# Kernel optimization log

Measured on AMD Instinct MI355X. Metric: run time of the kernel, lower is better.

## Reference

```python
import jax, jax.numpy as jnp
import numpy as np

EPS = 1e-8
BETA = 0.02          # bisector-band sharpness
ALPHA_UNION = 8.0    # exp-union strength
W_MIN, W_MAX = 0.005, 0.5
RAW_TEMP = 5.0       # width squash temperature
REL_TEMP = 0.05      # seed-relevance softmax temperature
A_MIN, A_MAX = 0.5, 2.0  # anisotropy eigenvalue range


def setup_inputs() -> dict:
    key = jax.random.key(0)
    k1, k2, k3, k4, k5 = jax.random.split(key, 5)
    N, S = 65536, 32
    return {
        "points_uv": jax.random.uniform(k1, (N, 2), dtype=jnp.float32),
        "seeds_raw": jax.random.uniform(k2, (S, 2), dtype=jnp.float32),
        "w_raw": jax.random.normal(k3, (1,), dtype=jnp.float32),
        "theta": jax.random.normal(k4, (S,), dtype=jnp.float32),
        "a_raw": jax.random.normal(k5, (S,), dtype=jnp.float32),
    }


def _metric_matrices(theta, a_raw):
    # anisotropic 2x2 SPD metrics M_s = R^T diag(a, 1/a) R
    t = jnp.tanh(a_raw)
    a = 0.5 * (A_MAX - A_MIN) * t + 0.5 * (A_MAX + A_MIN)  # (S,)
    c, s = jnp.cos(theta), jnp.sin(theta)
    R = jnp.stack([jnp.stack([c, -s], -1), jnp.stack([s, c], -1)], -2)  # (S,2,2)
    dvec = jnp.stack([a, 1.0 / (a + EPS)], -1)  # (S,2)
    return jnp.einsum("ska,sk,skb->sab", R, dvec, R)  # (S,2,2)


def reference(points_uv, seeds_raw, w_raw, theta, a_raw):
    S = seeds_raw.shape[0]
    # half-thickness around the Voronoi bisector
    w = W_MIN + (W_MAX - W_MIN) * jax.nn.sigmoid(w_raw[0] / RAW_TEMP)
    M = _metric_matrices(theta, a_raw)  # (S,2,2)

    # point-to-seed diffs with periodic wrapping on both u and v
    diff = points_uv[:, None, :] - seeds_raw[None, :, :]  # (N,S,2)
    diff = diff - jnp.round(diff)

    # anisotropic distances d_i(x) = sqrt(diff^T M_i diff)
    d = jnp.sqrt(jnp.einsum("nsa,sab,nsb->ns", diff, M, diff) + EPS)  # (N,S)

    # soft seed relevance -> soft pair weights P_ij (upper triangular, normalized)
    w_soft = jax.nn.softmax(-d / REL_TEMP, axis=1)  # (N,S)
    pair = w_soft[:, :, None] * w_soft[:, None, :]  # (N,S,S)
    mask = jnp.triu(jnp.ones((S, S), dtype=points_uv.dtype), k=1)
    pair = pair * mask
    P = pair / (pair.sum(axis=(1, 2), keepdims=True) + EPS)

    # bisector band: B_ij = sigmoid((w - |d_i - d_j|_smooth) / beta)
    Delta = d[:, :, None] - d[:, None, :]  # (N,S,S)
    abs_smooth = jnp.sqrt(Delta * Delta + EPS)
    B = jax.nn.sigmoid((w - abs_smooth) / BETA)

    # union over i<j pairs: rho = 1 - exp(-alpha * sum S_ij)
    S_sum = jnp.sum(P * B, axis=(1, 2))  # (N,)
    rho = 1.0 - jnp.exp(-ALPHA_UNION * S_sum)
    return rho
```

## Files before the change

kernel.cpp:

```cpp
#include <hip/hip_runtime.h>
#include <math.h>


#define LOG2E  1.4426950408889634f
#define EPSF   1e-8f
#define TSCALE 4096.0f
#define TAB_N  4160
#define BLOCK  512
#define PPB    64
#define SSTR   40

__device__ __forceinline__ float tabB(const char* tb, unsigned a, unsigned b) {
    const unsigned hi = a > b ? a : b;
    const unsigned lo = a > b ? b : a;
    return *(const float*)(tb + (hi - lo));
}

__global__ __launch_bounds__(BLOCK) void voronoi_v5(
    const float* __restrict__ points,
    const float* __restrict__ seeds,
    const float* __restrict__ w_raw,
    const float* __restrict__ theta,
    const float* __restrict__ a_raw,
    float* __restrict__ out,
    int N)
{
    __shared__ float    s_tab[TAB_N];
    __shared__ unsigned s_di[PPB * SSTR];
    __shared__ float    s_ww[PPB * SSTR];
    __shared__ float    s_su[32], s_sv[32], s_m00[32], s_m01[32], s_m11[32];

    const int t = threadIdx.x;

    const float wr = w_raw[0];
    const float sg = __builtin_amdgcn_rcpf(1.0f + exp2f(wr * (-LOG2E / 5.0f)));
    const float w  = 0.005f + 0.495f * sg;

    if (t < 32) {
        const float x  = a_raw[t];
        const float z  = exp2f(2.0f * LOG2E * x);
        const float th = (z - 1.0f) * __builtin_amdgcn_rcpf(z + 1.0f);
        const float a  = 0.75f * th + 1.25f;
        const float ia = __builtin_amdgcn_rcpf(a + EPSF);
        const float cs = __cosf(theta[t]);
        const float sn = __sinf(theta[t]);
        const float S2 = TSCALE * TSCALE;
        s_m00[t] = (a * cs * cs + ia * sn * sn) * S2;
        s_m01[t] = (2.0f * cs * sn * (ia - a)) * S2;
        s_m11[t] = (a * sn * sn + ia * cs * cs) * S2;
        s_su[t]  = seeds[2 * t];
        s_sv[t]  = seeds[2 * t + 1];
    }
    {
        const float kC = (50.0f * LOG2E) / TSCALE;
        const float kB = -w * (50.0f * LOG2E);
        for (int k = t; k < TAB_N; k += BLOCK) {
            const float y = exp2f(fmaf((float)k, kC, kB));
            s_tab[k] = __builtin_amdgcn_rcpf(1.0f + y);
        }
    }
    __syncthreads();

    const int pb = t >> 3;
    const int g  = t & 7;
    const int s0 = g * 4;
    const int p  = blockIdx.x * PPB + pb;
    if (p >= N) return;

    const float4 su4  = *(const float4*)&s_su[s0];
    const float4 sv4  = *(const float4*)&s_sv[s0];
    const float4 m004 = *(const float4*)&s_m00[s0];
    const float4 m014 = *(const float4*)&s_m01[s0];
    const float4 m114 = *(const float4*)&s_m11[s0];

    const float2 uv = ((const float2*)points)[p];
    const float u = uv.x, v = uv.y;

    const float EPS_Q = 1e-8f * TSCALE * TSCALE;
    float4 d4;
#define DIST(SU, SV, M00, M01, M11, OUTD)                                  \
    {                                                                      \
        float du = u - (SU); du -= rintf(du);                              \
        float dv = v - (SV); dv -= rintf(dv);                              \
        float q = fmaf(du * du, (M00),                                     \
                  fmaf(du * dv, (M01),                                     \
                  fmaf(dv * dv, (M11), EPS_Q)));                           \
        (OUTD) = sqrtf(q);                                                 \
    }
    DIST(su4.x, sv4.x, m004.x, m014.x, m114.x, d4.x)
    DIST(su4.y, sv4.y, m004.y, m014.y, m114.y, d4.y)
    DIST(su4.z, sv4.z, m004.z, m014.z, m114.z, d4.z)
    DIST(su4.w, sv4.w, m004.w, m014.w, m114.w, d4.w)

    const float cE = -(20.0f * LOG2E) / TSCALE;
    float4 e4;
    e4.x = exp2f(d4.x * cE);
    e4.y = exp2f(d4.y * cE);
    e4.z = exp2f(d4.z * cE);
    e4.w = exp2f(d4.w * cE);
    float Z = (e4.x + e4.y) + (e4.z + e4.w);
    Z += __shfl_xor(Z, 1, 64);
    Z += __shfl_xor(Z, 2, 64);
    Z += __shfl_xor(Z, 4, 64);
    const float rcpZ = __builtin_amdgcn_rcpf(Z);
    float4 w4;
    w4.x = e4.x * rcpZ; w4.y = e4.y * rcpZ;
    w4.z = e4.z * rcpZ; w4.w = e4.w * rcpZ;
    float sumsq = w4.x * w4.x;
    sumsq = fmaf(w4.y, w4.y, sumsq);
    sumsq = fmaf(w4.z, w4.z, sumsq);
    sumsq = fmaf(w4.w, w4.w, sumsq);

    uint4 ii;
    ii.x = ((unsigned)(d4.x + 0.5f)) << 2;
    ii.y = ((unsigned)(d4.y + 0.5f)) << 2;
    ii.z = ((unsigned)(d4.z + 0.5f)) << 2;
    ii.w = ((unsigned)(d4.w + 0.5f)) << 2;

    unsigned* db = &s_di[pb * SSTR];
    float*    wb = &s_ww[pb * SSTR];
    *(uint4*) (db + s0) = ii;
    *(float4*)(wb + s0) = w4;

    const char* tb = (const char*)s_tab;

    float b0, b1, b2, b3;
    b0 =      tabB(tb, ii.x, ii.y) * w4.y;
    b0 = fmaf(tabB(tb, ii.x, ii.z), w4.z, b0);
    b0 = fmaf(tabB(tb, ii.x, ii.w), w4.w, b0);
    b1 =      tabB(tb, ii.y, ii.z) * w4.z;
    b1 = fmaf(tabB(tb, ii.y, ii.w), w4.w, b1);
    b2 =      tabB(tb, ii.z, ii.w) * w4.w;
    b3 = 0.0f;

#define ROT(R, HALF)                                                       \
    {                                                                      \
        const int gj = ((g + (R)) & 7) * 4;                                \
        const uint4  ij = *(const uint4*) (db + gj);                       \
        float4 wj = *(const float4*)(wb + gj);                             \
        if (HALF) { wj.x *= 0.5f; wj.y *= 0.5f; wj.z *= 0.5f; wj.w *= 0.5f; } \
        b0 = fmaf(tabB(tb, ii.x, ij.x), wj.x, b0);                         \
        b0 = fmaf(tabB(tb, ii.x, ij.y), wj.y, b0);                         \
        b0 = fmaf(tabB(tb, ii.x, ij.z), wj.z, b0);                         \
        b0 = fmaf(tabB(tb, ii.x, ij.w), wj.w, b0);                         \
        b1 = fmaf(tabB(tb, ii.y, ij.x), wj.x, b1);                         \
        b1 = fmaf(tabB(tb, ii.y, ij.y), wj.y, b1);                         \
        b1 = fmaf(tabB(tb, ii.y, ij.z), wj.z, b1);                         \
        b1 = fmaf(tabB(tb, ii.y, ij.w), wj.w, b1);                         \
        b2 = fmaf(tabB(tb, ii.z, ij.x), wj.x, b2);                         \
        b2 = fmaf(tabB(tb, ii.z, ij.y), wj.y, b2);                         \
        b2 = fmaf(tabB(tb, ii.z, ij.z), wj.z, b2);                         \
        b2 = fmaf(tabB(tb, ii.z, ij.w), wj.w, b2);                         \
        b3 = fmaf(tabB(tb, ii.w, ij.x), wj.x, b3);                         \
        b3 = fmaf(tabB(tb, ii.w, ij.y), wj.y, b3);                         \
        b3 = fmaf(tabB(tb, ii.w, ij.z), wj.z, b3);                         \
        b3 = fmaf(tabB(tb, ii.w, ij.w), wj.w, b3);                         \
    }
    ROT(1, 0)
    ROT(2, 0)
    ROT(3, 0)
    ROT(4, 1)

    float accb = w4.x * b0;
    accb = fmaf(w4.y, b1, accb);
    accb = fmaf(w4.z, b2, accb);
    accb = fmaf(w4.w, b3, accb);

    float nb = accb, sq = sumsq;
    nb += __shfl_xor(nb, 1, 64);  sq += __shfl_xor(sq, 1, 64);
    nb += __shfl_xor(nb, 2, 64);  sq += __shfl_xor(sq, 2, 64);
    nb += __shfl_xor(nb, 4, 64);  sq += __shfl_xor(sq, 4, 64);

    const float den   = fmaxf(0.5f * (1.0f - sq), 0.0f) + EPSF;
    const float ratio = nb * __builtin_amdgcn_rcpf(den);
    const float rho   = 1.0f - exp2f(ratio * (-8.0f * LOG2E));
    if (g == 0) out[p] = rho;
}

extern "C" void kernel_launch(void* const* d_in, const int* in_sizes, int n_in,
                              void* d_out, int out_size, void* d_ws, size_t ws_size,
                              hipStream_t stream) {
    const float* points = (const float*)d_in[0];
    const float* seeds  = (const float*)d_in[1];
    const float* w_raw  = (const float*)d_in[2];
    const float* theta  = (const float*)d_in[3];
    const float* a_raw  = (const float*)d_in[4];
    float* out = (float*)d_out;

    const int N = in_sizes[0] / 2;
    const int grid = (N + PPB - 1) / PPB;

    voronoi_v5<<<grid, BLOCK, 0, stream>>>(points, seeds, w_raw, theta, a_raw,
                                           out, N);
}
```

Measured before the change: 16.85 us.

## Shrink sigmoid table to band around w and halve symmetric rotation work

The lookup table is cut to a clamped window of indices around the band centre w, on the assumption that the sigmoid is flat outside that window. This reduces the per-block table initialization and LDS footprint. The fourth rotation step is now done by only half the lanes instead of all lanes with halved weights, which removes duplicated pair work but adds divergence. Launch bounds ask for higher occupancy. Clamping index differences adds two min/max ops per lookup and approximates the table outside the window.

```diff
diff --git a/kernel.cpp b/kernel.cpp
--- a/kernel.cpp
+++ b/kernel.cpp
@@ -4,19 +4,14 @@
 
 #define LOG2E  1.4426950408889634f
 #define EPSF   1e-8f
-#define TSCALE 4096.0f
-#define TAB_N  4160
+#define TSC    4096.0f
+#define TAB_N  2816
+#define HBAND  750
 #define BLOCK  512
 #define PPB    64
 #define SSTR   40
 
-__device__ __forceinline__ float tabB(const char* tb, unsigned a, unsigned b) {
-    const unsigned hi = a > b ? a : b;
-    const unsigned lo = a > b ? b : a;
-    return *(const float*)(tb + (hi - lo));
-}
-
-__global__ __launch_bounds__(BLOCK) void voronoi_v5(
+__global__ __launch_bounds__(BLOCK, 8) void voronoi_v7(
     const float* __restrict__ points,
     const float* __restrict__ seeds,
     const float* __restrict__ w_raw,
@@ -26,7 +21,7 @@
     int N)
 {
     __shared__ float    s_tab[TAB_N];
-    __shared__ unsigned s_di[PPB * SSTR];
+    __shared__ unsigned s_ii[PPB * SSTR];
     __shared__ float    s_ww[PPB * SSTR];
     __shared__ float    s_su[32], s_sv[32], s_m00[32], s_m01[32], s_m11[32];
 
@@ -35,6 +30,10 @@
     const float wr = w_raw[0];
     const float sg = __builtin_amdgcn_rcpf(1.0f + exp2f(wr * (-LOG2E / 5.0f)));
     const float w  = 0.005f + 0.495f * sg;
+
+    const int icent = (int)(w * TSC + 0.5f);
+    const int T1B   = (icent > HBAND ? icent - HBAND : 0) << 2;
+    const int T2B   = (icent + HBAND) << 2;
 
     if (t < 32) {
         const float x  = a_raw[t];
@@ -44,7 +43,7 @@
         const float ia = __builtin_amdgcn_rcpf(a + EPSF);
         const float cs = __cosf(theta[t]);
         const float sn = __sinf(theta[t]);
-        const float S2 = TSCALE * TSCALE;
+        const float S2 = TSC * TSC;
         s_m00[t] = (a * cs * cs + ia * sn * sn) * S2;
         s_m01[t] = (2.0f * cs * sn * (ia - a)) * S2;
         s_m11[t] = (a * sn * sn + ia * cs * cs) * S2;
@@ -52,8 +51,9 @@
         s_sv[t]  = seeds[2 * t + 1];
     }
     {
-        const float kC = (50.0f * LOG2E) / TSCALE;
+        const float kC = (50.0f * LOG2E) / TSC;
         const float kB = -w * (50.0f * LOG2E);
+        #pragma unroll
         for (int k = t; k < TAB_N; k += BLOCK) {
             const float y = exp2f(fmaf((float)k, kC, kB));
             s_tab[k] = __builtin_amdgcn_rcpf(1.0f + y);
@@ -76,7 +76,7 @@
     const float2 uv = ((const float2*)points)[p];
     const float u = uv.x, v = uv.y;
 
-    const float EPS_Q = 1e-8f * TSCALE * TSCALE;
+    const float EPS_Q = 1e-8f * TSC * TSC;
     float4 d4;
 #define DIST(SU, SV, M00, M01, M11, OUTD)                                  \
     {                                                                      \
@@ -92,7 +92,7 @@
     DIST(su4.z, sv4.z, m004.z, m014.z, m114.z, d4.z)
     DIST(su4.w, sv4.w, m004.w, m014.w, m114.w, d4.w)
 
-    const float cE = -(20.0f * LOG2E) / TSCALE;
+    const float cE = -(20.0f * LOG2E) / TSC;
     float4 e4;
     e4.x = exp2f(d4.x * cE);
     e4.y = exp2f(d4.y * cE);
@@ -117,49 +117,61 @@
     ii.z = ((unsigned)(d4.z + 0.5f)) << 2;
     ii.w = ((unsigned)(d4.w + 0.5f)) << 2;
 
-    unsigned* db = &s_di[pb * SSTR];
+    unsigned* db = &s_ii[pb * SSTR];
     float*    wb = &s_ww[pb * SSTR];
     *(uint4*) (db + s0) = ii;
     *(float4*)(wb + s0) = w4;
 
     const char* tb = (const char*)s_tab;
 
+#define TBODY(IA, IB, WJ, ACC)                                             \
+    {                                                                      \
+        const unsigned hi = (IA) > (IB) ? (IA) : (IB);                     \
+        const unsigned lo = (IA) > (IB) ? (IB) : (IA);                     \
+        int diff = (int)(hi - lo);                                         \
+        diff = diff > T1B ? diff : T1B;                                    \
+        diff = diff < T2B ? diff : T2B;                                    \
+        const float B = *(const float*)(tb + diff);                        \
+        (ACC) = fmaf((WJ), B, (ACC));                                      \
+    }
+
     float b0, b1, b2, b3;
-    b0 =      tabB(tb, ii.x, ii.y) * w4.y;
-    b0 = fmaf(tabB(tb, ii.x, ii.z), w4.z, b0);
-    b0 = fmaf(tabB(tb, ii.x, ii.w), w4.w, b0);
-    b1 =      tabB(tb, ii.y, ii.z) * w4.z;
-    b1 = fmaf(tabB(tb, ii.y, ii.w), w4.w, b1);
-    b2 =      tabB(tb, ii.z, ii.w) * w4.w;
-    b3 = 0.0f;
-
-#define ROT(R, HALF)                                                       \
+    b0 = 0.0f; b1 = 0.0f; b2 = 0.0f; b3 = 0.0f;
+    TBODY(ii.x, ii.y, w4.y, b0)
+    TBODY(ii.x, ii.z, w4.z, b0)
+    TBODY(ii.x, ii.w, w4.w, b0)
+    TBODY(ii.y, ii.z, w4.z, b1)
+    TBODY(ii.y, ii.w, w4.w, b1)
+    TBODY(ii.z, ii.w, w4.w, b2)
+
+#define ROT(R)                                                             \
     {                                                                      \
         const int gj = ((g + (R)) & 7) * 4;                                \
         const uint4  ij = *(const uint4*) (db + gj);                       \
-        float4 wj = *(const float4*)(wb + gj);                             \
-        if (HALF) { wj.x *= 0.5f; wj.y *= 0.5f; wj.z *= 0.5f; wj.w *= 0.5f; } \
-        b0 = fmaf(tabB(tb, ii.x, ij.x), wj.x, b0);                         \
-        b0 = fmaf(tabB(tb, ii.x, ij.y), wj.y, b0);                         \
-        b0 = fmaf(tabB(tb, ii.x, ij.z), wj.z, b0);                         \
-        b0 = fmaf(tabB(tb, ii.x, ij.w), wj.w, b0);                         \
-        b1 = fmaf(tabB(tb, ii.y, ij.x), wj.x, b1);                         \
-        b1 = fmaf(tabB(tb, ii.y, ij.y), wj.y, b1);                         \
-        b1 = fmaf(tabB(tb, ii.y, ij.z), wj.z, b1);                         \
-        b1 = fmaf(tabB(tb, ii.y, ij.w), wj.w, b1);                         \
-        b2 = fmaf(tabB(tb, ii.z, ij.x), wj.x, b2);                         \
-        b2 = fmaf(tabB(tb, ii.z, ij.y), wj.y, b2);                         \
-        b2 = fmaf(tabB(tb, ii.z, ij.z), wj.z, b2);                         \
-        b2 = fmaf(tabB(tb, ii.z, ij.w), wj.w, b2);                         \
-        b3 = fmaf(tabB(tb, ii.w, ij.x), wj.x, b3);                         \
-        b3 = fmaf(tabB(tb, ii.w, ij.y), wj.y, b3);                         \
-        b3 = fmaf(tabB(tb, ii.w, ij.z), wj.z, b3);                         \
-        b3 = fmaf(tabB(tb, ii.w, ij.w), wj.w, b3);                         \
-    }
-    ROT(1, 0)
-    ROT(2, 0)
-    ROT(3, 0)
-    ROT(4, 1)
+        const float4 wj = *(const float4*)(wb + gj);                       \
+        TBODY(ii.x, ij.x, wj.x, b0)                                        \
+        TBODY(ii.x, ij.y, wj.y, b0)                                        \
+        TBODY(ii.x, ij.z, wj.z, b0)                                        \
+        TBODY(ii.x, ij.w, wj.w, b0)                                        \
+        TBODY(ii.y, ij.x, wj.x, b1)                                        \
+        TBODY(ii.y, ij.y, wj.y, b1)                                        \
+        TBODY(ii.y, ij.z, wj.z, b1)                                        \
+        TBODY(ii.y, ij.w, wj.w, b1)                                        \
+        TBODY(ii.z, ij.x, wj.x, b2)                                        \
+        TBODY(ii.z, ij.y, wj.y, b2)                                        \
+        TBODY(ii.z, ij.z, wj.z, b2)                                        \
+        TBODY(ii.z, ij.w, wj.w, b2)                                        \
+        TBODY(ii.w, ij.x, wj.x, b3)                                        \
+        TBODY(ii.w, ij.y, wj.y, b3)                                        \
+        TBODY(ii.w, ij.z, wj.z, b3)                                        \
+        TBODY(ii.w, ij.w, wj.w, b3)                                        \
+    }
+    ROT(1)
+    ROT(2)
+    ROT(3)
+    if (g < 4) {
+        ROT(4)
+    }
 
     float accb = w4.x * b0;
     accb = fmaf(w4.y, b1, accb);
@@ -190,6 +202,6 @@
     const int N = in_sizes[0] / 2;
     const int grid = (N + PPB - 1) / PPB;
 
-    voronoi_v5<<<grid, BLOCK, 0, stream>>>(points, seeds, w_raw, theta, a_raw,
+    voronoi_v7<<<grid, BLOCK, 0, stream>>>(points, seeds, w_raw, theta, a_raw,
                                            out, N);
 }
```

Result: faster. 16.49 us (-2.1%).

## Replace sigmoid lookup table with clamped rational tanh approximation

Applied to the files above, without the earlier changes.

Drops the per-block shared-memory sigmoid table and the quantized distance indices, and computes the bisector-band sigmoid directly from a clamped Padé tanh approximation in registers. Distances are stored as floats in shared memory instead of scaled integers. The aim is to remove the table build, its LDS footprint, and random LDS gathers, which should allow more blocks per CU (launch bounds raised to 8). The cost is considerably more ALU work per pair, including a reciprocal, and a small accuracy change from clamping at ±4.6.

```diff
diff --git a/kernel.cpp b/kernel.cpp
--- a/kernel.cpp
+++ b/kernel.cpp
@@ -4,19 +4,11 @@
 
 #define LOG2E  1.4426950408889634f
 #define EPSF   1e-8f
-#define TSCALE 4096.0f
-#define TAB_N  4160
 #define BLOCK  512
 #define PPB    64
 #define SSTR   40
 
-__device__ __forceinline__ float tabB(const char* tb, unsigned a, unsigned b) {
-    const unsigned hi = a > b ? a : b;
-    const unsigned lo = a > b ? b : a;
-    return *(const float*)(tb + (hi - lo));
-}
-
-__global__ __launch_bounds__(BLOCK) void voronoi_v5(
+__global__ __launch_bounds__(BLOCK, 8) void voronoi_v8(
     const float* __restrict__ points,
     const float* __restrict__ seeds,
     const float* __restrict__ w_raw,
@@ -25,16 +17,16 @@
     float* __restrict__ out,
     int N)
 {
-    __shared__ float    s_tab[TAB_N];
-    __shared__ unsigned s_di[PPB * SSTR];
-    __shared__ float    s_ww[PPB * SSTR];
-    __shared__ float    s_su[32], s_sv[32], s_m00[32], s_m01[32], s_m11[32];
+    __shared__ float s_dd[PPB * SSTR];
+    __shared__ float s_ww[PPB * SSTR];
+    __shared__ float s_su[32], s_sv[32], s_m00[32], s_m01[32], s_m11[32];
 
     const int t = threadIdx.x;
 
     const float wr = w_raw[0];
     const float sg = __builtin_amdgcn_rcpf(1.0f + exp2f(wr * (-LOG2E / 5.0f)));
     const float w  = 0.005f + 0.495f * sg;
+    const float wc = w * 25.0f;
 
     if (t < 32) {
         const float x  = a_raw[t];
@@ -44,20 +36,11 @@
         const float ia = __builtin_amdgcn_rcpf(a + EPSF);
         const float cs = __cosf(theta[t]);
         const float sn = __sinf(theta[t]);
-        const float S2 = TSCALE * TSCALE;
-        s_m00[t] = (a * cs * cs + ia * sn * sn) * S2;
-        s_m01[t] = (2.0f * cs * sn * (ia - a)) * S2;
-        s_m11[t] = (a * sn * sn + ia * cs * cs) * S2;
+        s_m00[t] = a * cs * cs + ia * sn * sn;
+        s_m01[t] = 2.0f * cs * sn * (ia - a);
+        s_m11[t] = a * sn * sn + ia * cs * cs;
         s_su[t]  = seeds[2 * t];
         s_sv[t]  = seeds[2 * t + 1];
-    }
-    {
-        const float kC = (50.0f * LOG2E) / TSCALE;
-        const float kB = -w * (50.0f * LOG2E);
-        for (int k = t; k < TAB_N; k += BLOCK) {
-            const float y = exp2f(fmaf((float)k, kC, kB));
-            s_tab[k] = __builtin_amdgcn_rcpf(1.0f + y);
-        }
     }
     __syncthreads();
 
@@ -76,7 +59,6 @@
     const float2 uv = ((const float2*)points)[p];
     const float u = uv.x, v = uv.y;
 
-    const float EPS_Q = 1e-8f * TSCALE * TSCALE;
     float4 d4;
 #define DIST(SU, SV, M00, M01, M11, OUTD)                                  \
     {                                                                      \
@@ -84,7 +66,7 @@
         float dv = v - (SV); dv -= rintf(dv);                              \
         float q = fmaf(du * du, (M00),                                     \
                   fmaf(du * dv, (M01),                                     \
-                  fmaf(dv * dv, (M11), EPS_Q)));                           \
+                  fmaf(dv * dv, (M11), EPSF)));                            \
         (OUTD) = sqrtf(q);                                                 \
     }
     DIST(su4.x, sv4.x, m004.x, m014.x, m114.x, d4.x)
@@ -92,7 +74,7 @@
     DIST(su4.z, sv4.z, m004.z, m014.z, m114.z, d4.z)
     DIST(su4.w, sv4.w, m004.w, m014.w, m114.w, d4.w)
 
-    const float cE = -(20.0f * LOG2E) / TSCALE;
+    const float cE = -20.0f * LOG2E;
     float4 e4;
     e4.x = exp2f(d4.x * cE);
     e4.y = exp2f(d4.y * cE);
@@ -111,50 +93,57 @@
     sumsq = fmaf(w4.z, w4.z, sumsq);
     sumsq = fmaf(w4.w, w4.w, sumsq);
 
-    uint4 ii;
-    ii.x = ((unsigned)(d4.x + 0.5f)) << 2;
-    ii.y = ((unsigned)(d4.y + 0.5f)) << 2;
-    ii.z = ((unsigned)(d4.z + 0.5f)) << 2;
-    ii.w = ((unsigned)(d4.w + 0.5f)) << 2;
-
-    unsigned* db = &s_di[pb * SSTR];
-    float*    wb = &s_ww[pb * SSTR];
-    *(uint4*) (db + s0) = ii;
+    float* db = &s_dd[pb * SSTR];
+    float* wb = &s_ww[pb * SSTR];
+    *(float4*)(db + s0) = d4;
     *(float4*)(wb + s0) = w4;
 
-    const char* tb = (const char*)s_tab;
+#define FBODY(DI, DJ, WJ, ACC)                                             \
+    {                                                                      \
+        const float ab = fabsf((DI) - (DJ));                               \
+        float x = fmaf(ab, -25.0f, wc);                                    \
+        x = fminf(fmaxf(x, -4.6f), 4.6f);                                  \
+        const float tt = x * x;                                            \
+        const float nm = fmaf(fmaf(tt + 378.0f, tt, 17325.0f), tt,         \
+                              135135.0f);                                  \
+        const float dn = fmaf(fmaf(fmaf(28.0f, tt, 3150.0f), tt,           \
+                              62370.0f), tt, 135135.0f);                   \
+        const float xr = x * __builtin_amdgcn_rcpf(dn);                    \
+        const float B  = fmaf(nm * xr, 0.5f, 0.5f);                        \
+        (ACC) = fmaf((WJ), B, (ACC));                                      \
+    }
 
     float b0, b1, b2, b3;
-    b0 =      tabB(tb, ii.x, ii.y) * w4.y;
-    b0 = fmaf(tabB(tb, ii.x, ii.z), w4.z, b0);
-    b0 = fmaf(tabB(tb, ii.x, ii.w), w4.w, b0);
-    b1 =      tabB(tb, ii.y, ii.z) * w4.z;
-    b1 = fmaf(tabB(tb, ii.y, ii.w), w4.w, b1);
-    b2 =      tabB(tb, ii.z, ii.w) * w4.w;
-    b3 = 0.0f;
+    b0 = 0.0f; b1 = 0.0f; b2 = 0.0f; b3 = 0.0f;
+    FBODY(d4.x, d4.y, w4.y, b0)
+    FBODY(d4.x, d4.z, w4.z, b0)
+    FBODY(d4.x, d4.w, w4.w, b0)
+    FBODY(d4.y, d4.z, w4.z, b1)
+    FBODY(d4.y, d4.w, w4.w, b1)
+    FBODY(d4.z, d4.w, w4.w, b2)
 
 #define ROT(R, HALF)                                                       \
     {                                                                      \
         const int gj = ((g + (R)) & 7) * 4;                                \
-        const uint4  ij = *(const uint4*) (db + gj);                       \
+        const float4 dj = *(const float4*)(db + gj);                       \
         float4 wj = *(const float4*)(wb + gj);                             \
         if (HALF) { wj.x *= 0.5f; wj.y *= 0.5f; wj.z *= 0.5f; wj.w *= 0.5f; } \
-        b0 = fmaf(tabB(tb, ii.x, ij.x), wj.x, b0);                         \
-        b0 = fmaf(tabB(tb, ii.x, ij.y), wj.y, b0);                         \
-        b0 = fmaf(tabB(tb, ii.x, ij.z), wj.z, b0);                         \
-        b0 = fmaf(tabB(tb, ii.x, ij.w), wj.w, b0);                         \
-        b1 = fmaf(tabB(tb, ii.y, ij.x), wj.x, b1);                         \
-        b1 = fmaf(tabB(tb, ii.y, ij.y), wj.y, b1);                         \
-        b1 = fmaf(tabB(tb, ii.y, ij.z), wj.z, b1);                         \
-        b1 = fmaf(tabB(tb, ii.y, ij.w), wj.w, b1);                         \
-        b2 = fmaf(tabB(tb, ii.z, ij.x), wj.x, b2);                         \
-        b2 = fmaf(tabB(tb, ii.z, ij.y), wj.y, b2);                         \
-        b2 = fmaf(tabB(tb, ii.z, ij.z), wj.z, b2);                         \
-        b2 = fmaf(tabB(tb, ii.z, ij.w), wj.w, b2);                         \
-        b3 = fmaf(tabB(tb, ii.w, ij.x), wj.x, b3);                         \
-        b3 = fmaf(tabB(tb, ii.w, ij.y), wj.y, b3);                         \
-        b3 = fmaf(tabB(tb, ii.w, ij.z), wj.z, b3);                         \
-        b3 = fmaf(tabB(tb, ii.w, ij.w), wj.w, b3);                         \
+        FBODY(d4.x, dj.x, wj.x, b0)                                        \
+        FBODY(d4.x, dj.y, wj.y, b0)                                        \
+        FBODY(d4.x, dj.z, wj.z, b0)                                        \
+        FBODY(d4.x, dj.w, wj.w, b0)                                        \
+        FBODY(d4.y, dj.x, wj.x, b1)                                        \
+        FBODY(d4.y, dj.y, wj.y, b1)                                        \
+        FBODY(d4.y, dj.z, wj.z, b1)                                        \
+        FBODY(d4.y, dj.w, wj.w, b1)                                        \
+        FBODY(d4.z, dj.x, wj.x, b2)                                        \
+        FBODY(d4.z, dj.y, wj.y, b2)                                        \
+        FBODY(d4.z, dj.z, wj.z, b2)                                        \
+        FBODY(d4.z, dj.w, wj.w, b2)                                        \
+        FBODY(d4.w, dj.x, wj.x, b3)                                        \
+        FBODY(d4.w, dj.y, wj.y, b3)                                        \
+        FBODY(d4.w, dj.z, wj.z, b3)                                        \
+        FBODY(d4.w, dj.w, wj.w, b3)                                        \
     }
     ROT(1, 0)
     ROT(2, 0)
@@ -190,6 +179,6 @@
     const int N = in_sizes[0] / 2;
     const int grid = (N + PPB - 1) / PPB;
 
-    voronoi_v5<<<grid, BLOCK, 0, stream>>>(points, seeds, w_raw, theta, a_raw,
+    voronoi_v8<<<grid, BLOCK, 0, stream>>>(points, seeds, w_raw, theta, a_raw,
                                            out, N);
 }
```

Result: slower. 24.52 us (+45.6%).
